# Kernel optimization log

Measured on AMD Instinct MI355X. Metric: run time of the kernel, lower is better.

The kernel has to match this reference:

```python
import jax, jax.numpy as jnp
import numpy as np

B, GEO_CH, SEM_CH, H, W = 8, 256, 256, 64, 64
HS, WS = 32, 32  # semantic branch spatial size
EPS_ATTN = 1e-6
EPS_GN = 1e-5


def _phi(x):
    return jax.nn.elu(x) + 1.0


def setup_inputs() -> dict:
    key = jax.random.key(0)
    ks = jax.random.split(key, 8)
    f_geo = jax.random.normal(ks[0], (B, GEO_CH, H, W), dtype=jnp.float32)
    f_sem = jax.random.normal(ks[1], (B, SEM_CH, HS, WS), dtype=jnp.float32)
    s = 0.02
    Wq = jax.random.normal(ks[2], (SEM_CH, GEO_CH), dtype=jnp.float32) * s
    Wk = jax.random.normal(ks[3], (SEM_CH, SEM_CH), dtype=jnp.float32) * s
    Wv = jax.random.normal(ks[4], (SEM_CH, SEM_CH), dtype=jnp.float32) * s
    Wo = jax.random.normal(ks[5], (GEO_CH, SEM_CH), dtype=jnp.float32) * s
    bq = jnp.zeros((SEM_CH,), jnp.float32)
    bk = jnp.zeros((SEM_CH,), jnp.float32)
    bv = jnp.zeros((SEM_CH,), jnp.float32)
    bo = jnp.zeros((GEO_CH,), jnp.float32)
    gn_w = jnp.ones((GEO_CH,), jnp.float32)
    gn_b = jnp.zeros((GEO_CH,), jnp.float32)
    return {"f_geo": f_geo, "f_sem": f_sem, "Wq": Wq, "bq": bq, "Wk": Wk,
            "bk": bk, "Wv": Wv, "bv": bv, "Wo": Wo, "bo": bo,
            "gn_w": gn_w, "gn_b": gn_b}


def _conv1x1(x, Wm, b):
    # x: [B,Cin,H,W], Wm: [Cout,Cin] -> [B,Cout,H,W]
    return jnp.einsum('oc,bchw->bohw', Wm, x) + b[None, :, None, None]


def reference(f_geo, f_sem, Wq, bq, Wk, bk, Wv, bv, Wo, bo, gn_w, gn_b):
    b, cg, h, w = f_geo.shape
    n = h * w
    # bilinear resize, half-pixel centers == torch align_corners=False
    f_sem_r = jax.image.resize(f_sem, (b, f_sem.shape[1], h, w), method='bilinear')
    Q = _phi(_conv1x1(f_geo, Wq, bq)).reshape(b, -1, n)      # [B,Cs,N]
    K = _phi(_conv1x1(f_sem_r, Wk, bk)).reshape(b, -1, n)    # [B,Cs,N]
    V = _conv1x1(f_sem_r, Wv, bv).reshape(b, -1, n)          # [B,Cs,N]
    KV = jnp.einsum('bcn,bdn->bcd', K, V)                    # [B,Cs,Cs]
    QKV = jnp.einsum('bcn,bcd->bnd', Q, KV)                  # [B,N,Cs]
    K_sum = K.sum(axis=-1)                                   # [B,Cs]
    norm = jnp.einsum('bcn,bc->bn', Q, K_sum)[..., None] + EPS_ATTN  # [B,N,1]
    out = (QKV / norm).transpose(0, 2, 1).reshape(b, -1, h, w)
    y = f_geo + _conv1x1(out, Wo, bo)
    # GroupNorm(1, geo_ch): normalize over (C,H,W) per sample, per-channel affine
    mu = y.mean(axis=(1, 2, 3), keepdims=True)
    var = y.var(axis=(1, 2, 3), keepdims=True)
    yn = (y - mu) * jax.lax.rsqrt(var + EPS_GN)
    return yn * gn_w[None, :, None, None] + gn_b[None, :, None, None]
```

## Files before the change

kernel.cpp:

```cpp
#include <hip/hip_runtime.h>
#include <hip/hip_bf16.h>


#define B_ 8
#define C_ 256
#define N_ 4096
#define NS_ 1024
#define KVCH 16

typedef unsigned short u16;
using bf16x8 = __attribute__((ext_vector_type(8))) short;
using f32x4 = __attribute__((ext_vector_type(4))) float;

__device__ inline u16 f2bf(float f) {
  unsigned u = __builtin_bit_cast(unsigned, f);
  unsigned r = (u + 0x7fffu + ((u >> 16) & 1u)) >> 16;
  return (u16)r;
}
__device__ inline float bf2f(u16 x) {
  return __builtin_bit_cast(float, ((unsigned)x) << 16);
}

__device__ __forceinline__ void gl_lds16(const u16* g, u16* l) {
  __builtin_amdgcn_global_load_lds((const __attribute__((address_space(1))) void*)g,
                                   (__attribute__((address_space(3))) void*)l, 16, 0, 0);
}

__device__ inline void gemm128_nt(const u16* __restrict__ At, const u16* __restrict__ Bt,
                                  int lda, int ldb, int k0, int k1,
                                  u16* __restrict__ lds, f32x4 acc[4][4])
{
  const int t = threadIdx.x;
  const int lane = t & 63, wave = t >> 6;
  const int wr = wave >> 1, wc = wave & 1;
  const int lr = lane & 15, lg = lane >> 4;
  const int sr = t >> 2, skv = (t & 3) * 8;
  u16* Ab = lds;
  u16* Bb = lds + 128 * 32;
  const u16* gA0 = At + (size_t)sr * lda + skv;
  const u16* gA1 = At + (size_t)(sr + 64) * lda + skv;
  const u16* gB0 = Bt + (size_t)sr * ldb + skv;
  const u16* gB1 = Bt + (size_t)(sr + 64) * ldb + skv;
  u16* dA0 = Ab + wave * 512;
  u16* dA1 = Ab + 2048 + wave * 512;
  u16* dB0 = Bb + wave * 512;
  u16* dB1 = Bb + 2048 + wave * 512;
  const u16* ap = Ab + (wr * 64 + lr) * 32 + lg * 8;
  const u16* bp = Bb + (wc * 64 + lr) * 32 + lg * 8;
  for (int k = k0; k < k1; k += 32) {
    gl_lds16(gA0 + k, dA0);
    gl_lds16(gA1 + k, dA1);
    gl_lds16(gB0 + k, dB0);
    gl_lds16(gB1 + k, dB1);
    __syncthreads();
    bf16x8 af[4], bfr[4];
#pragma unroll
    for (int i = 0; i < 4; ++i) af[i] = *reinterpret_cast<const bf16x8*>(ap + i * 16 * 32);
#pragma unroll
    for (int i = 0; i < 4; ++i) bfr[i] = *reinterpret_cast<const bf16x8*>(bp + i * 16 * 32);
#pragma unroll
    for (int m = 0; m < 4; ++m)
#pragma unroll
      for (int n = 0; n < 4; ++n)
        acc[m][n] = __builtin_amdgcn_mfma_f32_16x16x32_bf16(af[m], bfr[n], acc[m][n], 0, 0, 0);
    __syncthreads();
  }
}

__device__ inline void zero_acc4(f32x4 acc[4][4]) {
#pragma unroll
  for (int m = 0; m < 4; ++m)
#pragma unroll
    for (int n = 0; n < 4; ++n)
#pragma unroll
      for (int r = 0; r < 4; ++r) acc[m][n][r] = 0.f;
}

__device__ inline void ep_stage_half(const f32x4 acc[4][4], float* eplds, int h,
                                     int wr, int wc, int lr, int lg)
{
  if (wr == h) {
#pragma unroll
    for (int m = 0; m < 4; ++m)
#pragma unroll
      for (int n = 0; n < 4; ++n)
#pragma unroll
        for (int r = 0; r < 4; ++r)
          eplds[(m * 16 + lg * 4 + r) * 132 + wc * 64 + n * 16 + lr] = acc[m][n][r];
  }
}

__global__ __launch_bounds__(256) void k_transpose_cast(const float* __restrict__ in,
                                                        u16* __restrict__ out, int rows, int cols)
{
  __shared__ float tile[32][33];
  int b = blockIdx.z;
  const float* src = in + (size_t)b * rows * cols;
  u16* dst = out + (size_t)b * rows * cols;
  int c0 = blockIdx.x * 32, r0 = blockIdx.y * 32;
  int tx = threadIdx.x & 31, ty = threadIdx.x >> 5;
#pragma unroll
  for (int i = 0; i < 32; i += 8)
    tile[ty + i][tx] = src[(size_t)(r0 + ty + i) * cols + (c0 + tx)];
  __syncthreads();
#pragma unroll
  for (int i = 0; i < 32; i += 8)
    dst[(size_t)(c0 + ty + i) * rows + (r0 + tx)] = f2bf(tile[tx][ty + i]);
}

__global__ __launch_bounds__(256) void k_cast3(const float* __restrict__ wq, const float* __restrict__ wk,
                                               const float* __restrict__ wo,
                                               u16* oq, u16* ok, u16* oo,
                                               const float* __restrict__ bv, float* __restrict__ bov,
                                               float* __restrict__ stats)
{
  int i = blockIdx.x * 256 + threadIdx.x;
  oq[i] = f2bf(wq[i]); ok[i] = f2bf(wk[i]); oo[i] = f2bf(wo[i]);
  if (i < 16) stats[i] = 0.f;
  if (blockIdx.x == 255) {
    int o = threadIdx.x;
    float s = 0.f;
    for (int d = 0; d < C_; ++d) s += wo[o * C_ + d] * bv[d];
    bov[o] = s;
  }
}

__global__ __launch_bounds__(256) void k_wov(const u16* __restrict__ Wob, const u16* __restrict__ WvT,
                                             u16* __restrict__ Wov)
{
  __shared__ u16 glds[2 * 128 * 32];
  __shared__ float eplds[64 * 132];
  int tn = blockIdx.x, tm = blockIdx.y;
  const u16* A = Wob + (size_t)tm * 128 * C_;
  const u16* Bm = WvT + (size_t)tn * 128 * C_;
  f32x4 acc[4][4];
  zero_acc4(acc);
  gemm128_nt(A, Bm, C_, C_, 0, C_, glds, acc);
  int t = threadIdx.x, lane = t & 63, wave = t >> 6;
  int wr = wave >> 1, wc = wave & 1, lr = lane & 15, lg = lane >> 4;
  for (int h = 0; h < 2; ++h) {
    __syncthreads();
    ep_stage_half(acc, eplds, h, wr, wc, lr, lg);
    __syncthreads();
#pragma unroll
    for (int p = 0; p < 4; ++p) {
      int rloc = p * 8 + (t >> 5), cloc = (t & 31) * 4;
      int row = tm * 128 + h * 64 + rloc;
      float4 a = *(const float4*)&eplds[rloc * 132 + cloc];
      ushort4 o;
      o.x = f2bf(a.x); o.y = f2bf(a.y); o.z = f2bf(a.z); o.w = f2bf(a.w);
      *(ushort4*)&Wov[(size_t)row * C_ + tn * 128 + cloc] = o;
    }
  }
}

__global__ __launch_bounds__(256) void k_semconv(const u16* __restrict__ fsemT,
                                                 const u16* __restrict__ Wk, const u16* __restrict__ Wov,
                                                 const float* __restrict__ bk, const float* __restrict__ bov,
                                                 u16* __restrict__ Kpre, u16* __restrict__ V2pre)
{
  __shared__ u16 glds[2 * 128 * 32];
  __shared__ float eplds[64 * 132];
  int b = blockIdx.z >> 1, sel = blockIdx.z & 1;
  int m0 = blockIdx.y * 128, n0 = blockIdx.x * 128;
  const u16* A = (sel ? Wov : Wk) + (size_t)m0 * C_;
  const u16* Bm = fsemT + (size_t)b * NS_ * C_ + (size_t)n0 * C_;
  const float* bias = sel ? bov : bk;
  u16* out = (sel ? V2pre : Kpre) + (size_t)b * C_ * NS_;
  f32x4 acc[4][4];
  zero_acc4(acc);
  gemm128_nt(A, Bm, C_, C_, 0, C_, glds, acc);
  int t = threadIdx.x, lane = t & 63, wave = t >> 6;
  int wr = wave >> 1, wc = wave & 1, lr = lane & 15, lg = lane >> 4;
  for (int h = 0; h < 2; ++h) {
    __syncthreads();
    ep_stage_half(acc, eplds, h, wr, wc, lr, lg);
    __syncthreads();
#pragma unroll
    for (int p = 0; p < 4; ++p) {
      int rloc = p * 8 + (t >> 5), cloc = (t & 31) * 4;
      int row = m0 + h * 64 + rloc;
      float4 a = *(const float4*)&eplds[rloc * 132 + cloc];
      float bi = bias[row];
      ushort4 o;
      o.x = f2bf(a.x + bi); o.y = f2bf(a.y + bi); o.z = f2bf(a.z + bi); o.w = f2bf(a.w + bi);
      *(ushort4*)&out[(size_t)row * NS_ + n0 + cloc] = o;
    }
  }
}

__global__ __launch_bounds__(256) void k_resize(const u16* __restrict__ Kpre, const u16* __restrict__ V2pre,
                                                u16* __restrict__ Kbf, u16* __restrict__ V2bf,
                                                float* __restrict__ Ksum)
{
  int sel = blockIdx.y;
  const u16* src = (sel ? V2pre : Kpre) + (size_t)blockIdx.x * NS_;
  u16* dst = (sel ? V2bf : Kbf) + (size_t)blockIdx.x * N_;
  float s = 0.f;
  for (int i = threadIdx.x; i < N_; i += 256) {
    int yy = i >> 6, xx = i & 63;
    int yh = yy >> 1, xh = xx >> 1;
    int ys0, ys1, xs0, xs1; float wy0, wy1, wx0, wx1;
    if (yy & 1) { ys0 = yh; ys1 = yh < 31 ? yh + 1 : 31; wy0 = 0.75f; wy1 = 0.25f; }
    else        { ys0 = yh > 0 ? yh - 1 : 0; ys1 = yh;   wy0 = 0.25f; wy1 = 0.75f; }
    if (xx & 1) { xs0 = xh; xs1 = xh < 31 ? xh + 1 : 31; wx0 = 0.75f; wx1 = 0.25f; }
    else        { xs0 = xh > 0 ? xh - 1 : 0; xs1 = xh;   wx0 = 0.25f; wx1 = 0.75f; }
    float r0 = wx0 * bf2f(src[ys0 * 32 + xs0]) + wx1 * bf2f(src[ys0 * 32 + xs1]);
    float r1 = wx0 * bf2f(src[ys1 * 32 + xs0]) + wx1 * bf2f(src[ys1 * 32 + xs1]);
    float v = wy0 * r0 + wy1 * r1;
    if (!sel) { v = v > 0.f ? v + 1.f : __expf(v); s += v; }
    dst[i] = f2bf(v);
  }
  if (!sel) {
    __shared__ float red[256];
    red[threadIdx.x] = s; __syncthreads();
    for (int off = 128; off > 0; off >>= 1) {
      if (threadIdx.x < off) red[threadIdx.x] += red[threadIdx.x + off];
      __syncthreads();
    }
    if (threadIdx.x == 0) Ksum[blockIdx.x] = red[0];
  }
}

__global__ __launch_bounds__(256) void k_kv(const u16* __restrict__ V2bf, const u16* __restrict__ Kbf,
                                            float* __restrict__ Mpart)
{
  __shared__ u16 glds[2 * 128 * 32];
  __shared__ float eplds[64 * 132];
  int tn = blockIdx.x, tm = blockIdx.y;
  int b = blockIdx.z >> 4, ch = blockIdx.z & 15;
  const int kspan = N_ / KVCH;
  const u16* A = V2bf + (size_t)b * C_ * N_ + (size_t)tm * 128 * N_;
  const u16* Bm = Kbf + (size_t)b * C_ * N_ + (size_t)tn * 128 * N_;
  f32x4 acc[4][4];
  zero_acc4(acc);
  gemm128_nt(A, Bm, N_, N_, ch * kspan, ch * kspan + kspan, glds, acc);
  float* out = Mpart + ((size_t)(b * KVCH + ch) * 4 + tm * 2 + tn) * (128 * 128);
  int t = threadIdx.x, lane = t & 63, wave = t >> 6;
  int wr = wave >> 1, wc = wave & 1, lr = lane & 15, lg = lane >> 4;
  for (int h = 0; h < 2; ++h) {
    __syncthreads();
    ep_stage_half(acc, eplds, h, wr, wc, lr, lg);
    __syncthreads();
#pragma unroll
    for (int p = 0; p < 4; ++p) {
      int rloc = p * 8 + (t >> 5), cloc = (t & 31) * 4;
      float4 a = *(const float4*)&eplds[rloc * 132 + cloc];
      *(float4*)&out[(size_t)(h * 64 + rloc) * 128 + cloc] = a;
    }
    __syncthreads();
  }
}

__global__ __launch_bounds__(256) void k_kvred(const float* __restrict__ Mpart, u16* __restrict__ Mbf)
{
  int idx = blockIdx.x * 256 + threadIdx.x;
  int b = idx >> 16, cd = idx & 65535;
  int o = cd >> 8, c = cd & 255;
  int tile = ((o >> 7) << 1) + (c >> 7);
  int loc = (o & 127) * 128 + (c & 127);
  float s = 0.f;
#pragma unroll
  for (int ch = 0; ch < KVCH; ++ch)
    s += Mpart[((size_t)(b * KVCH + ch) * 4 + tile) * 16384 + loc];
  Mbf[idx] = f2bf(s);
}

__global__ __launch_bounds__(256) void k_fuse(const u16* __restrict__ fgeoT, const u16* __restrict__ Wqb,
                                              const float* __restrict__ bq, const float* __restrict__ Ksum,
                                              const u16* __restrict__ Mbf,
                                              const float* __restrict__ fgeo, const float* __restrict__ bo,
                                              float* __restrict__ y, float* __restrict__ stats)
{
  __shared__ u16 Qlds[64 * 264];
  __shared__ float normLds[64];
  __shared__ u16 stage[4096];
  __shared__ float eplds[32 * 68];
  const int t = threadIdx.x, lane = t & 63, wave = t >> 6;
  const int wr = wave >> 1, wc = wave & 1;
  const int lr = lane & 15, lg = lane >> 4;
  const int sr = t >> 2, skv = (t & 3) * 8;
  const int n0 = blockIdx.x * 64, b = blockIdx.y;
  if (t < 64) normLds[t] = 1e-6f;

  const u16* gA1 = fgeoT + (size_t)b * N_ * C_ + (size_t)(n0 + sr) * C_ + skv;
  for (int cc = 0; cc < 4; ++cc) {
    f32x4 a1[2][2];
#pragma unroll
    for (int m = 0; m < 2; ++m)
#pragma unroll
      for (int n = 0; n < 2; ++n)
#pragma unroll
        for (int r = 0; r < 4; ++r) a1[m][n][r] = 0.f;
    const u16* gB1 = Wqb + (size_t)(cc * 64 + sr) * C_ + skv;
    for (int k = 0; k < C_; k += 32) {
      gl_lds16(gA1 + k, stage + wave * 512);
      gl_lds16(gB1 + k, stage + 2048 + wave * 512);
      __syncthreads();
      const u16* ap = stage + (wr * 32 + lr) * 32 + lg * 8;
      const u16* bp = stage + 2048 + (wc * 32 + lr) * 32 + lg * 8;
      bf16x8 af[2], bfr[2];
#pragma unroll
      for (int i = 0; i < 2; ++i) af[i] = *(const bf16x8*)(ap + i * 16 * 32);
#pragma unroll
      for (int i = 0; i < 2; ++i) bfr[i] = *(const bf16x8*)(bp + i * 16 * 32);
#pragma unroll
      for (int m = 0; m < 2; ++m)
#pragma unroll
        for (int n = 0; n < 2; ++n)
          a1[m][n] = __builtin_amdgcn_mfma_f32_16x16x32_bf16(af[m], bfr[n], a1[m][n], 0, 0, 0);
      __syncthreads();
    }
#pragma unroll
    for (int m = 0; m < 2; ++m)
#pragma unroll
      for (int r = 0; r < 4; ++r) {
        int rown = wr * 32 + m * 16 + lg * 4 + r;
        float pn = 0.f;
#pragma unroll
        for (int n = 0; n < 2; ++n) {
          int colg = cc * 64 + wc * 32 + n * 16 + lr;
          float v = a1[m][n][r] + bq[colg];
          v = v > 0.f ? v + 1.f : __expf(v);
          Qlds[rown * 264 + colg] = f2bf(v);
          pn += v * Ksum[b * C_ + colg];
        }
        pn += __shfl_xor(pn, 1); pn += __shfl_xor(pn, 2);
        pn += __shfl_xor(pn, 4); pn += __shfl_xor(pn, 8);
        if (lr == 0) atomicAdd(&normLds[rown], pn);
      }
  }

  const float* fg = fgeo + (size_t)b * C_ * N_;
  float* yb = y + (size_t)b * C_ * N_;
  float ssum = 0.f, ssq = 0.f;
  for (int oh = 0; oh < 2; ++oh) {
    f32x4 a2[4][2];
#pragma unroll
    for (int m = 0; m < 4; ++m)
#pragma unroll
      for (int n = 0; n < 2; ++n)
#pragma unroll
        for (int r = 0; r < 4; ++r) a2[m][n][r] = 0.f;
    const u16* gM = Mbf + (size_t)b * C_ * C_ + (size_t)(oh * 128 + sr) * C_ + skv;
    for (int k = 0; k < C_; k += 32) {
      gl_lds16(gM + k, stage + wave * 512);
      gl_lds16(gM + (size_t)64 * C_ + k, stage + 2048 + wave * 512);
      __syncthreads();
      const u16* ap = stage + (wr * 64 + lr) * 32 + lg * 8;
      bf16x8 af[4], bfr[2];
#pragma unroll
      for (int i = 0; i < 4; ++i) af[i] = *(const bf16x8*)(ap + i * 16 * 32);
#pragma unroll
      for (int i = 0; i < 2; ++i)
        bfr[i] = *(const bf16x8*)&Qlds[(wc * 32 + i * 16 + lr) * 264 + k + lg * 8];
#pragma unroll
      for (int m = 0; m < 4; ++m)
#pragma unroll
        for (int n = 0; n < 2; ++n)
          a2[m][n] = __builtin_amdgcn_mfma_f32_16x16x32_bf16(af[m], bfr[n], a2[m][n], 0, 0, 0);
      __syncthreads();
    }
    for (int q = 0; q < 4; ++q) {
      __syncthreads();
      if (wr == (q >> 1)) {
        int m0 = (q & 1) * 2;
#pragma unroll
        for (int mm = 0; mm < 2; ++mm)
#pragma unroll
          for (int n = 0; n < 2; ++n)
#pragma unroll
            for (int r = 0; r < 4; ++r)
              eplds[(mm * 16 + lg * 4 + r) * 68 + wc * 32 + n * 16 + lr] = a2[m0 + mm][n][r];
      }
      __syncthreads();
#pragma unroll
      for (int p = 0; p < 2; ++p) {
        int rloc = p * 16 + (t >> 4), cloc = (t & 15) * 4;
        int o = oh * 128 + q * 32 + rloc;
        float4 a = *(const float4*)&eplds[rloc * 68 + cloc];
        float4 nv = *(const float4*)&normLds[cloc];
        float4 f = *(const float4*)&fg[(size_t)o * N_ + n0 + cloc];
        float bov = bo[o];
        float4 v;
        v.x = f.x + bov + a.x / nv.x;
        v.y = f.y + bov + a.y / nv.y;
        v.z = f.z + bov + a.z / nv.z;
        v.w = f.w + bov + a.w / nv.w;
        *(float4*)&yb[(size_t)o * N_ + n0 + cloc] = v;
        ssum += v.x + v.y + v.z + v.w;
        ssq += v.x * v.x + v.y * v.y + v.z * v.z + v.w * v.w;
      }
    }
  }
#pragma unroll
  for (int off = 1; off < 64; off <<= 1) {
    ssum += __shfl_xor(ssum, off);
    ssq += __shfl_xor(ssq, off);
  }
  if (lane == 0) {
    atomicAdd(&stats[b * 2], ssum);
    atomicAdd(&stats[b * 2 + 1], ssq);
  }
}

__global__ __launch_bounds__(256) void k_gn(float* __restrict__ y, const float* __restrict__ stats,
                                            const float* __restrict__ gnw, const float* __restrict__ gnb)
{
  int idx = blockIdx.x * 256 + threadIdx.x;
  int elem = idx * 8;
  int b = elem >> 20;
  int o = (elem >> 12) & 255;
  const float cnt = (float)C_ * (float)N_;
  float mu = stats[b * 2] / cnt;
  float var = stats[b * 2 + 1] / cnt - mu * mu;
  float rs = rsqrtf(var + 1e-5f);
  float sc = gnw[o] * rs;
  float sh = gnb[o] - mu * sc;
  float4* p = reinterpret_cast<float4*>(y) + idx * 2;
  float4 v0 = p[0], v1 = p[1];
  v0.x = v0.x * sc + sh; v0.y = v0.y * sc + sh; v0.z = v0.z * sc + sh; v0.w = v0.w * sc + sh;
  v1.x = v1.x * sc + sh; v1.y = v1.y * sc + sh; v1.z = v1.z * sc + sh; v1.w = v1.w * sc + sh;
  p[0] = v0; p[1] = v1;
}

extern "C" void kernel_launch(void* const* d_in, const int* in_sizes, int n_in,
                              void* d_out, int out_size, void* d_ws, size_t ws_size,
                              hipStream_t stream)
{
  const float* f_geo = (const float*)d_in[0];
  const float* f_sem = (const float*)d_in[1];
  const float* Wq = (const float*)d_in[2];
  const float* bq = (const float*)d_in[3];
  const float* Wk = (const float*)d_in[4];
  const float* bk = (const float*)d_in[5];
  const float* Wv = (const float*)d_in[6];
  const float* bv = (const float*)d_in[7];
  const float* Wo = (const float*)d_in[8];
  const float* bo = (const float*)d_in[9];
  const float* gnw = (const float*)d_in[10];
  const float* gnb = (const float*)d_in[11];
  float* y = (float*)d_out;

  char* w = (char*)d_ws;
  auto alloc = [&](size_t bytes) { char* p = w; w += (bytes + 255) & ~(size_t)255; return p; };
  u16* fsemT = (u16*)alloc((size_t)B_ * NS_ * C_ * 2);
  u16* fgeoT = (u16*)alloc((size_t)B_ * N_ * C_ * 2);
  u16* Wqb = (u16*)alloc(65536 * 2);
  u16* Wkb = (u16*)alloc(65536 * 2);
  u16* Wob = (u16*)alloc(65536 * 2);
  u16* WvT = (u16*)alloc(65536 * 2);
  u16* Wov = (u16*)alloc(65536 * 2);
  float* bov = (float*)alloc(C_ * 4);
  u16* Kpre = (u16*)alloc((size_t)B_ * C_ * NS_ * 2);
  u16* V2pre = (u16*)alloc((size_t)B_ * C_ * NS_ * 2);
  u16* Kbf = (u16*)alloc((size_t)B_ * C_ * N_ * 2);
  u16* V2bf = (u16*)alloc((size_t)B_ * C_ * N_ * 2);
  float* Ksum = (float*)alloc((size_t)B_ * C_ * 4);
  float* Mpart = (float*)alloc((size_t)B_ * KVCH * 4 * 16384 * 4);
  u16* Mbf = (u16*)alloc((size_t)B_ * C_ * C_ * 2);
  float* stats = (float*)alloc(256);

  k_transpose_cast<<<dim3(NS_ / 32, C_ / 32, B_), 256, 0, stream>>>(f_sem, fsemT, C_, NS_);
  k_transpose_cast<<<dim3(N_ / 32, C_ / 32, B_), 256, 0, stream>>>(f_geo, fgeoT, C_, N_);
  k_transpose_cast<<<dim3(C_ / 32, C_ / 32, 1), 256, 0, stream>>>(Wv, WvT, C_, C_);
  k_cast3<<<dim3(256), 256, 0, stream>>>(Wq, Wk, Wo, Wqb, Wkb, Wob, bv, bov, stats);
  k_wov<<<dim3(2, 2), 256, 0, stream>>>(Wob, WvT, Wov);
  k_semconv<<<dim3(8, 2, 16), 256, 0, stream>>>(fsemT, Wkb, Wov, bk, bov, Kpre, V2pre);
  k_resize<<<dim3(B_ * C_, 2), 256, 0, stream>>>(Kpre, V2pre, Kbf, V2bf, Ksum);
  k_kv<<<dim3(2, 2, B_ * KVCH), 256, 0, stream>>>(V2bf, Kbf, Mpart);
  k_kvred<<<dim3(2048), 256, 0, stream>>>(Mpart, Mbf);
  k_fuse<<<dim3(N_ / 64, B_), 256, 0, stream>>>(fgeoT, Wqb, bq, Ksum, Mbf, f_geo, bo, y, stats);
  k_gn<<<dim3(B_ * C_ * N_ / 8 / 256), 256, 0, stream>>>(y, stats, gnw, gnb);
}
```

Before: 277.2 us.

## Shrink GEMM tiles to 64x64 with deeper K staging and retile fused attention kernel

Replaces the 128x128 GEMM helper with a 64x64 tile that stages 128-wide K slabs per barrier. k_wov, k_semconv and k_kv are relaunched with four times more blocks, and their LDS is aliased between staging and epilogue. k_kvred is vectorized with float4. k_fuse now works on 32-pixel tiles, keeps the Q operand fragments in registers and streams Wq and M in 32-row chunks, aiming for more parallelism and fewer barriers at the cost of more redundant weight loads per block.

New measurement: 322.8 us. +16.4%, slower.

```diff
diff --git a/kernel.cpp b/kernel.cpp
--- a/kernel.cpp
+++ b/kernel.cpp
@@ -20,73 +20,44 @@
 __device__ inline float bf2f(u16 x) {
   return __builtin_bit_cast(float, ((unsigned)x) << 16);
 }
-
 __device__ __forceinline__ void gl_lds16(const u16* g, u16* l) {
   __builtin_amdgcn_global_load_lds((const __attribute__((address_space(1))) void*)g,
                                    (__attribute__((address_space(3))) void*)l, 16, 0, 0);
 }
 
-__device__ inline void gemm128_nt(const u16* __restrict__ At, const u16* __restrict__ Bt,
-                                  int lda, int ldb, int k0, int k1,
-                                  u16* __restrict__ lds, f32x4 acc[4][4])
-{
-  const int t = threadIdx.x;
-  const int lane = t & 63, wave = t >> 6;
-  const int wr = wave >> 1, wc = wave & 1;
-  const int lr = lane & 15, lg = lane >> 4;
-  const int sr = t >> 2, skv = (t & 3) * 8;
-  u16* Ab = lds;
-  u16* Bb = lds + 128 * 32;
-  const u16* gA0 = At + (size_t)sr * lda + skv;
-  const u16* gA1 = At + (size_t)(sr + 64) * lda + skv;
-  const u16* gB0 = Bt + (size_t)sr * ldb + skv;
-  const u16* gB1 = Bt + (size_t)(sr + 64) * ldb + skv;
-  u16* dA0 = Ab + wave * 512;
-  u16* dA1 = Ab + 2048 + wave * 512;
-  u16* dB0 = Bb + wave * 512;
-  u16* dB1 = Bb + 2048 + wave * 512;
-  const u16* ap = Ab + (wr * 64 + lr) * 32 + lg * 8;
-  const u16* bp = Bb + (wc * 64 + lr) * 32 + lg * 8;
-  for (int k = k0; k < k1; k += 32) {
-    gl_lds16(gA0 + k, dA0);
-    gl_lds16(gA1 + k, dA1);
-    gl_lds16(gB0 + k, dB0);
-    gl_lds16(gB1 + k, dB1);
+__device__ inline void gemm64(const u16* __restrict__ A, const u16* __restrict__ Bm,
+                              int lda, int ldb, int k0,
+                              u16* __restrict__ lds, f32x4 (&acc)[2][2])
+{
+  const int t = threadIdx.x, lane = t & 63, w = t >> 6;
+  const int wr = w >> 1, wc = w & 1, lr = lane & 15;
+  const int lg = lane >> 4;
+  const int srow = w * 16 + (lane >> 2), scol = (lane & 3) * 8;
+  u16* Alds = lds;
+  u16* Blds = lds + 8192;
+  for (int slab = 0; slab < 2; ++slab) {
+    const int kb = k0 + slab * 128;
+#pragma unroll
+    for (int i = 0; i < 4; ++i)
+      gl_lds16(A + (size_t)srow * lda + kb + i * 32 + scol, Alds + i * 2048 + w * 512);
+#pragma unroll
+    for (int i = 0; i < 4; ++i)
+      gl_lds16(Bm + (size_t)srow * ldb + kb + i * 32 + scol, Blds + i * 2048 + w * 512);
     __syncthreads();
-    bf16x8 af[4], bfr[4];
-#pragma unroll
-    for (int i = 0; i < 4; ++i) af[i] = *reinterpret_cast<const bf16x8*>(ap + i * 16 * 32);
-#pragma unroll
-    for (int i = 0; i < 4; ++i) bfr[i] = *reinterpret_cast<const bf16x8*>(bp + i * 16 * 32);
-#pragma unroll
-    for (int m = 0; m < 4; ++m)
-#pragma unroll
-      for (int n = 0; n < 4; ++n)
-        acc[m][n] = __builtin_amdgcn_mfma_f32_16x16x32_bf16(af[m], bfr[n], acc[m][n], 0, 0, 0);
+#pragma unroll
+    for (int ch = 0; ch < 4; ++ch) {
+      const u16* ap = Alds + ch * 2048 + (wr * 32 + lr) * 32 + lg * 8;
+      const u16* bp = Blds + ch * 2048 + (wc * 32 + lr) * 32 + lg * 8;
+      bf16x8 af[2], bf[2];
+      af[0] = *(const bf16x8*)ap; af[1] = *(const bf16x8*)(ap + 16 * 32);
+      bf[0] = *(const bf16x8*)bp; bf[1] = *(const bf16x8*)(bp + 16 * 32);
+#pragma unroll
+      for (int m = 0; m < 2; ++m)
+#pragma unroll
+        for (int n = 0; n < 2; ++n)
+          acc[m][n] = __builtin_amdgcn_mfma_f32_16x16x32_bf16(af[m], bf[n], acc[m][n], 0, 0, 0);
+    }
     __syncthreads();
-  }
-}
-
-__device__ inline void zero_acc4(f32x4 acc[4][4]) {
-#pragma unroll
-  for (int m = 0; m < 4; ++m)
-#pragma unroll
-    for (int n = 0; n < 4; ++n)
-#pragma unroll
-      for (int r = 0; r < 4; ++r) acc[m][n][r] = 0.f;
-}
-
-__device__ inline void ep_stage_half(const f32x4 acc[4][4], float* eplds, int h,
-                                     int wr, int wc, int lr, int lg)
-{
-  if (wr == h) {
-#pragma unroll
-    for (int m = 0; m < 4; ++m)
-#pragma unroll
-      for (int n = 0; n < 4; ++n)
-#pragma unroll
-        for (int r = 0; r < 4; ++r)
-          eplds[(m * 16 + lg * 4 + r) * 132 + wc * 64 + n * 16 + lr] = acc[m][n][r];
   }
 }
 
@@ -128,29 +99,29 @@
 __global__ __launch_bounds__(256) void k_wov(const u16* __restrict__ Wob, const u16* __restrict__ WvT,
                                              u16* __restrict__ Wov)
 {
-  __shared__ u16 glds[2 * 128 * 32];
-  __shared__ float eplds[64 * 132];
+  __shared__ __align__(16) char smem[32768];
+  u16* glds = (u16*)smem;
+  float* eplds = (float*)smem;
   int tn = blockIdx.x, tm = blockIdx.y;
-  const u16* A = Wob + (size_t)tm * 128 * C_;
-  const u16* Bm = WvT + (size_t)tn * 128 * C_;
-  f32x4 acc[4][4];
-  zero_acc4(acc);
-  gemm128_nt(A, Bm, C_, C_, 0, C_, glds, acc);
-  int t = threadIdx.x, lane = t & 63, wave = t >> 6;
-  int wr = wave >> 1, wc = wave & 1, lr = lane & 15, lg = lane >> 4;
-  for (int h = 0; h < 2; ++h) {
-    __syncthreads();
-    ep_stage_half(acc, eplds, h, wr, wc, lr, lg);
-    __syncthreads();
-#pragma unroll
-    for (int p = 0; p < 4; ++p) {
-      int rloc = p * 8 + (t >> 5), cloc = (t & 31) * 4;
-      int row = tm * 128 + h * 64 + rloc;
-      float4 a = *(const float4*)&eplds[rloc * 132 + cloc];
-      ushort4 o;
-      o.x = f2bf(a.x); o.y = f2bf(a.y); o.z = f2bf(a.z); o.w = f2bf(a.w);
-      *(ushort4*)&Wov[(size_t)row * C_ + tn * 128 + cloc] = o;
-    }
+  f32x4 acc[2][2] = {};
+  gemm64(Wob + (size_t)tm * 64 * C_, WvT + (size_t)tn * 64 * C_, C_, C_, 0, glds, acc);
+  int t = threadIdx.x, lane = t & 63, w = t >> 6;
+  int wr = w >> 1, wc = w & 1, lr = lane & 15, lg = lane >> 4;
+#pragma unroll
+  for (int m = 0; m < 2; ++m)
+#pragma unroll
+    for (int n = 0; n < 2; ++n)
+#pragma unroll
+      for (int r = 0; r < 4; ++r)
+        eplds[(wr * 32 + m * 16 + lg * 4 + r) * 68 + wc * 32 + n * 16 + lr] = acc[m][n][r];
+  __syncthreads();
+#pragma unroll
+  for (int rd = 0; rd < 4; ++rd) {
+    int rloc = rd * 16 + (t >> 4), cloc = (t & 15) * 4;
+    float4 a = *(const float4*)&eplds[rloc * 68 + cloc];
+    ushort4 o;
+    o.x = f2bf(a.x); o.y = f2bf(a.y); o.z = f2bf(a.z); o.w = f2bf(a.w);
+    *(ushort4*)&Wov[(size_t)(tm * 64 + rloc) * C_ + tn * 64 + cloc] = o;
   }
 }
 
@@ -159,33 +130,36 @@
                                                  const float* __restrict__ bk, const float* __restrict__ bov,
                                                  u16* __restrict__ Kpre, u16* __restrict__ V2pre)
 {
-  __shared__ u16 glds[2 * 128 * 32];
-  __shared__ float eplds[64 * 132];
+  __shared__ __align__(16) char smem[32768];
+  u16* glds = (u16*)smem;
+  float* eplds = (float*)smem;
   int b = blockIdx.z >> 1, sel = blockIdx.z & 1;
-  int m0 = blockIdx.y * 128, n0 = blockIdx.x * 128;
+  int m0 = blockIdx.y * 64, n0 = blockIdx.x * 64;
   const u16* A = (sel ? Wov : Wk) + (size_t)m0 * C_;
   const u16* Bm = fsemT + (size_t)b * NS_ * C_ + (size_t)n0 * C_;
   const float* bias = sel ? bov : bk;
   u16* out = (sel ? V2pre : Kpre) + (size_t)b * C_ * NS_;
-  f32x4 acc[4][4];
-  zero_acc4(acc);
-  gemm128_nt(A, Bm, C_, C_, 0, C_, glds, acc);
-  int t = threadIdx.x, lane = t & 63, wave = t >> 6;
-  int wr = wave >> 1, wc = wave & 1, lr = lane & 15, lg = lane >> 4;
-  for (int h = 0; h < 2; ++h) {
-    __syncthreads();
-    ep_stage_half(acc, eplds, h, wr, wc, lr, lg);
-    __syncthreads();
-#pragma unroll
-    for (int p = 0; p < 4; ++p) {
-      int rloc = p * 8 + (t >> 5), cloc = (t & 31) * 4;
-      int row = m0 + h * 64 + rloc;
-      float4 a = *(const float4*)&eplds[rloc * 132 + cloc];
-      float bi = bias[row];
-      ushort4 o;
-      o.x = f2bf(a.x + bi); o.y = f2bf(a.y + bi); o.z = f2bf(a.z + bi); o.w = f2bf(a.w + bi);
-      *(ushort4*)&out[(size_t)row * NS_ + n0 + cloc] = o;
-    }
+  f32x4 acc[2][2] = {};
+  gemm64(A, Bm, C_, C_, 0, glds, acc);
+  int t = threadIdx.x, lane = t & 63, w = t >> 6;
+  int wr = w >> 1, wc = w & 1, lr = lane & 15, lg = lane >> 4;
+#pragma unroll
+  for (int m = 0; m < 2; ++m)
+#pragma unroll
+    for (int n = 0; n < 2; ++n)
+#pragma unroll
+      for (int r = 0; r < 4; ++r)
+        eplds[(wr * 32 + m * 16 + lg * 4 + r) * 68 + wc * 32 + n * 16 + lr] = acc[m][n][r];
+  __syncthreads();
+#pragma unroll
+  for (int rd = 0; rd < 4; ++rd) {
+    int rloc = rd * 16 + (t >> 4), cloc = (t & 15) * 4;
+    int row = m0 + rloc;
+    float4 a = *(const float4*)&eplds[rloc * 68 + cloc];
+    float bi = bias[row];
+    ushort4 o;
+    o.x = f2bf(a.x + bi); o.y = f2bf(a.y + bi); o.z = f2bf(a.z + bi); o.w = f2bf(a.w + bi);
+    *(ushort4*)&out[(size_t)row * NS_ + n0 + cloc] = o;
   }
 }
 
@@ -225,45 +199,53 @@
 __global__ __launch_bounds__(256) void k_kv(const u16* __restrict__ V2bf, const u16* __restrict__ Kbf,
                                             float* __restrict__ Mpart)
 {
-  __shared__ u16 glds[2 * 128 * 32];
-  __shared__ float eplds[64 * 132];
+  __shared__ __align__(16) char smem[32768];
+  u16* glds = (u16*)smem;
+  float* eplds = (float*)smem;
   int tn = blockIdx.x, tm = blockIdx.y;
   int b = blockIdx.z >> 4, ch = blockIdx.z & 15;
-  const int kspan = N_ / KVCH;
-  const u16* A = V2bf + (size_t)b * C_ * N_ + (size_t)tm * 128 * N_;
-  const u16* Bm = Kbf + (size_t)b * C_ * N_ + (size_t)tn * 128 * N_;
-  f32x4 acc[4][4];
-  zero_acc4(acc);
-  gemm128_nt(A, Bm, N_, N_, ch * kspan, ch * kspan + kspan, glds, acc);
-  float* out = Mpart + ((size_t)(b * KVCH + ch) * 4 + tm * 2 + tn) * (128 * 128);
-  int t = threadIdx.x, lane = t & 63, wave = t >> 6;
-  int wr = wave >> 1, wc = wave & 1, lr = lane & 15, lg = lane >> 4;
-  for (int h = 0; h < 2; ++h) {
-    __syncthreads();
-    ep_stage_half(acc, eplds, h, wr, wc, lr, lg);
-    __syncthreads();
-#pragma unroll
-    for (int p = 0; p < 4; ++p) {
-      int rloc = p * 8 + (t >> 5), cloc = (t & 31) * 4;
-      float4 a = *(const float4*)&eplds[rloc * 132 + cloc];
-      *(float4*)&out[(size_t)(h * 64 + rloc) * 128 + cloc] = a;
-    }
-    __syncthreads();
+  const u16* A = V2bf + (size_t)b * C_ * N_ + (size_t)tm * 64 * N_;
+  const u16* Bm = Kbf + (size_t)b * C_ * N_ + (size_t)tn * 64 * N_;
+  f32x4 acc[2][2] = {};
+  gemm64(A, Bm, N_, N_, ch * 256, glds, acc);
+  float* out = Mpart + ((size_t)(b * 16 + ch) * 16 + tm * 4 + tn) * 4096;
+  int t = threadIdx.x, lane = t & 63, w = t >> 6;
+  int wr = w >> 1, wc = w & 1, lr = lane & 15, lg = lane >> 4;
+#pragma unroll
+  for (int m = 0; m < 2; ++m)
+#pragma unroll
+    for (int n = 0; n < 2; ++n)
+#pragma unroll
+      for (int r = 0; r < 4; ++r)
+        eplds[(wr * 32 + m * 16 + lg * 4 + r) * 68 + wc * 32 + n * 16 + lr] = acc[m][n][r];
+  __syncthreads();
+#pragma unroll
+  for (int rd = 0; rd < 4; ++rd) {
+    int rloc = rd * 16 + (t >> 4), cloc = (t & 15) * 4;
+    float4 a = *(const float4*)&eplds[rloc * 68 + cloc];
+    *(float4*)&out[rloc * 64 + cloc] = a;
   }
 }
 
 __global__ __launch_bounds__(256) void k_kvred(const float* __restrict__ Mpart, u16* __restrict__ Mbf)
 {
-  int idx = blockIdx.x * 256 + threadIdx.x;
-  int b = idx >> 16, cd = idx & 65535;
-  int o = cd >> 8, c = cd & 255;
-  int tile = ((o >> 7) << 1) + (c >> 7);
-  int loc = (o & 127) * 128 + (c & 127);
-  float s = 0.f;
-#pragma unroll
-  for (int ch = 0; ch < KVCH; ++ch)
-    s += Mpart[((size_t)(b * KVCH + ch) * 4 + tile) * 16384 + loc];
-  Mbf[idx] = f2bf(s);
+  int q = blockIdx.x * 256 + threadIdx.x;
+  int b = q >> 14;
+  int rem = q & 16383;
+  int o = rem >> 6;
+  int c0 = (rem & 63) * 4;
+  int tile = ((o >> 6) << 2) + (c0 >> 6);
+  int loc = (o & 63) * 64 + (c0 & 63);
+  const float* base = Mpart + (size_t)b * 16 * 16 * 4096 + (size_t)tile * 4096 + loc;
+  float4 s = {0.f, 0.f, 0.f, 0.f};
+#pragma unroll
+  for (int ch = 0; ch < KVCH; ++ch) {
+    float4 v = *(const float4*)(base + (size_t)ch * 16 * 4096);
+    s.x += v.x; s.y += v.y; s.z += v.z; s.w += v.w;
+  }
+  ushort4 out;
+  out.x = f2bf(s.x); out.y = f2bf(s.y); out.z = f2bf(s.z); out.w = f2bf(s.w);
+  *(ushort4*)&Mbf[(size_t)q * 4] = out;
 }
 
 __global__ __launch_bounds__(256) void k_fuse(const u16* __restrict__ fgeoT, const u16* __restrict__ Wqb,
@@ -272,125 +254,104 @@
                                               const float* __restrict__ fgeo, const float* __restrict__ bo,
                                               float* __restrict__ y, float* __restrict__ stats)
 {
-  __shared__ u16 Qlds[64 * 264];
-  __shared__ float normLds[64];
-  __shared__ u16 stage[4096];
-  __shared__ float eplds[32 * 68];
-  const int t = threadIdx.x, lane = t & 63, wave = t >> 6;
-  const int wr = wave >> 1, wc = wave & 1;
-  const int lr = lane & 15, lg = lane >> 4;
-  const int sr = t >> 2, skv = (t & 3) * 8;
-  const int n0 = blockIdx.x * 64, b = blockIdx.y;
-  if (t < 64) normLds[t] = 1e-6f;
-
-  const u16* gA1 = fgeoT + (size_t)b * N_ * C_ + (size_t)(n0 + sr) * C_ + skv;
-  for (int cc = 0; cc < 4; ++cc) {
-    f32x4 a1[2][2];
-#pragma unroll
-    for (int m = 0; m < 2; ++m)
-#pragma unroll
-      for (int n = 0; n < 2; ++n)
-#pragma unroll
-        for (int r = 0; r < 4; ++r) a1[m][n][r] = 0.f;
-    const u16* gB1 = Wqb + (size_t)(cc * 64 + sr) * C_ + skv;
-    for (int k = 0; k < C_; k += 32) {
-      gl_lds16(gA1 + k, stage + wave * 512);
-      gl_lds16(gB1 + k, stage + 2048 + wave * 512);
+  __shared__ __align__(16) char smem[66688];
+  u16* Qlds = (u16*)smem;
+  u16* Ast = (u16*)(smem + 33792);
+  u16* Bst = (u16*)(smem + 50176);
+  float* normLds = (float*)(smem + 66560);
+  float* eplds = (float*)(smem + 33792);
+  const int t = threadIdx.x, lane = t & 63, w = t >> 6;
+  const int wr = w >> 1, wc = w & 1, lr = lane & 15, lg = lane >> 4;
+  const int sr2 = (w & 1) * 16 + (lane >> 2);
+  const int sch2 = w >> 1;
+  const int scol = (lane & 3) * 8;
+  const int n0 = blockIdx.x * 32, b = blockIdx.y;
+  if (t < 32) normLds[t] = 1e-6f;
+
+  auto stage32 = [&](const u16* g, u16* dst) {
+#pragma unroll
+    for (int i = 0; i < 4; ++i)
+      gl_lds16(g + (size_t)sr2 * C_ + (2 * i + sch2) * 32 + scol, dst + i * 2048 + w * 512);
+  };
+
+  stage32(fgeoT + (size_t)b * N_ * C_ + (size_t)n0 * C_, Ast);
+  stage32(Wqb, Bst);
+  __syncthreads();
+
+  float bqv[8], ksv[8];
+#pragma unroll
+  for (int cc = 0; cc < 8; ++cc) {
+    int c = cc * 32 + wc * 16 + lr;
+    bqv[cc] = bq[c];
+    ksv[cc] = Ksum[b * C_ + c];
+  }
+  bf16x8 af[8];
+#pragma unroll
+  for (int ch = 0; ch < 8; ++ch)
+    af[ch] = *(const bf16x8*)(Ast + ch * 1024 + (wr * 16 + lr) * 32 + lg * 8);
+
+  for (int cc = 0; cc < 8; ++cc) {
+    f32x4 a1 = {0.f, 0.f, 0.f, 0.f};
+#pragma unroll
+    for (int ch = 0; ch < 8; ++ch) {
+      bf16x8 bf = *(const bf16x8*)(Bst + ch * 1024 + (wc * 16 + lr) * 32 + lg * 8);
+      a1 = __builtin_amdgcn_mfma_f32_16x16x32_bf16(af[ch], bf, a1, 0, 0, 0);
+    }
+#pragma unroll
+    for (int rr = 0; rr < 4; ++rr) {
+      int n = wr * 16 + lg * 4 + rr;
+      float v = a1[rr] + bqv[cc];
+      v = v > 0.f ? v + 1.f : __expf(v);
+      Qlds[n * 264 + cc * 32 + wc * 16 + lr] = f2bf(v);
+      float pn = v * ksv[cc];
+      pn += __shfl_xor(pn, 1); pn += __shfl_xor(pn, 2);
+      pn += __shfl_xor(pn, 4); pn += __shfl_xor(pn, 8);
+      if (lr == 0) atomicAdd(&normLds[n], pn);
+    }
+    __syncthreads();
+    if (cc < 7) {
+      stage32(Wqb + (size_t)(cc + 1) * 32 * C_, Bst);
       __syncthreads();
-      const u16* ap = stage + (wr * 32 + lr) * 32 + lg * 8;
-      const u16* bp = stage + 2048 + (wc * 32 + lr) * 32 + lg * 8;
-      bf16x8 af[2], bfr[2];
-#pragma unroll
-      for (int i = 0; i < 2; ++i) af[i] = *(const bf16x8*)(ap + i * 16 * 32);
-#pragma unroll
-      for (int i = 0; i < 2; ++i) bfr[i] = *(const bf16x8*)(bp + i * 16 * 32);
-#pragma unroll
-      for (int m = 0; m < 2; ++m)
-#pragma unroll
-        for (int n = 0; n < 2; ++n)
-          a1[m][n] = __builtin_amdgcn_mfma_f32_16x16x32_bf16(af[m], bfr[n], a1[m][n], 0, 0, 0);
-      __syncthreads();
-    }
-#pragma unroll
-    for (int m = 0; m < 2; ++m)
-#pragma unroll
-      for (int r = 0; r < 4; ++r) {
-        int rown = wr * 32 + m * 16 + lg * 4 + r;
-        float pn = 0.f;
-#pragma unroll
-        for (int n = 0; n < 2; ++n) {
-          int colg = cc * 64 + wc * 32 + n * 16 + lr;
-          float v = a1[m][n][r] + bq[colg];
-          v = v > 0.f ? v + 1.f : __expf(v);
-          Qlds[rown * 264 + colg] = f2bf(v);
-          pn += v * Ksum[b * C_ + colg];
-        }
-        pn += __shfl_xor(pn, 1); pn += __shfl_xor(pn, 2);
-        pn += __shfl_xor(pn, 4); pn += __shfl_xor(pn, 8);
-        if (lr == 0) atomicAdd(&normLds[rown], pn);
-      }
-  }
+    }
+  }
+
+  __syncthreads();
+  bf16x8 qf[8];
+#pragma unroll
+  for (int ch = 0; ch < 8; ++ch)
+    qf[ch] = *(const bf16x8*)&Qlds[(wc * 16 + lr) * 264 + ch * 32 + lg * 8];
 
   const float* fg = fgeo + (size_t)b * C_ * N_;
   float* yb = y + (size_t)b * C_ * N_;
   float ssum = 0.f, ssq = 0.f;
-  for (int oh = 0; oh < 2; ++oh) {
-    f32x4 a2[4][2];
-#pragma unroll
-    for (int m = 0; m < 4; ++m)
-#pragma unroll
-      for (int n = 0; n < 2; ++n)
-#pragma unroll
-        for (int r = 0; r < 4; ++r) a2[m][n][r] = 0.f;
-    const u16* gM = Mbf + (size_t)b * C_ * C_ + (size_t)(oh * 128 + sr) * C_ + skv;
-    for (int k = 0; k < C_; k += 32) {
-      gl_lds16(gM + k, stage + wave * 512);
-      gl_lds16(gM + (size_t)64 * C_ + k, stage + 2048 + wave * 512);
-      __syncthreads();
-      const u16* ap = stage + (wr * 64 + lr) * 32 + lg * 8;
-      bf16x8 af[4], bfr[2];
-#pragma unroll
-      for (int i = 0; i < 4; ++i) af[i] = *(const bf16x8*)(ap + i * 16 * 32);
-#pragma unroll
-      for (int i = 0; i < 2; ++i)
-        bfr[i] = *(const bf16x8*)&Qlds[(wc * 32 + i * 16 + lr) * 264 + k + lg * 8];
-#pragma unroll
-      for (int m = 0; m < 4; ++m)
-#pragma unroll
-        for (int n = 0; n < 2; ++n)
-          a2[m][n] = __builtin_amdgcn_mfma_f32_16x16x32_bf16(af[m], bfr[n], a2[m][n], 0, 0, 0);
-      __syncthreads();
-    }
-    for (int q = 0; q < 4; ++q) {
-      __syncthreads();
-      if (wr == (q >> 1)) {
-        int m0 = (q & 1) * 2;
-#pragma unroll
-        for (int mm = 0; mm < 2; ++mm)
-#pragma unroll
-          for (int n = 0; n < 2; ++n)
-#pragma unroll
-            for (int r = 0; r < 4; ++r)
-              eplds[(mm * 16 + lg * 4 + r) * 68 + wc * 32 + n * 16 + lr] = a2[m0 + mm][n][r];
-      }
-      __syncthreads();
-#pragma unroll
-      for (int p = 0; p < 2; ++p) {
-        int rloc = p * 16 + (t >> 4), cloc = (t & 15) * 4;
-        int o = oh * 128 + q * 32 + rloc;
-        float4 a = *(const float4*)&eplds[rloc * 68 + cloc];
-        float4 nv = *(const float4*)&normLds[cloc];
-        float4 f = *(const float4*)&fg[(size_t)o * N_ + n0 + cloc];
-        float bov = bo[o];
-        float4 v;
-        v.x = f.x + bov + a.x / nv.x;
-        v.y = f.y + bov + a.y / nv.y;
-        v.z = f.z + bov + a.z / nv.z;
-        v.w = f.w + bov + a.w / nv.w;
-        *(float4*)&yb[(size_t)o * N_ + n0 + cloc] = v;
-        ssum += v.x + v.y + v.z + v.w;
-        ssq += v.x * v.x + v.y * v.y + v.z * v.z + v.w * v.w;
-      }
+  for (int oh = 0; oh < 8; ++oh) {
+    stage32(Mbf + (size_t)b * C_ * C_ + (size_t)oh * 32 * C_, Bst);
+    __syncthreads();
+    f32x4 a2 = {0.f, 0.f, 0.f, 0.f};
+#pragma unroll
+    for (int ch = 0; ch < 8; ++ch) {
+      bf16x8 mf = *(const bf16x8*)(Bst + ch * 1024 + (wr * 16 + lr) * 32 + lg * 8);
+      a2 = __builtin_amdgcn_mfma_f32_16x16x32_bf16(mf, qf[ch], a2, 0, 0, 0);
+    }
+#pragma unroll
+    for (int rr = 0; rr < 4; ++rr)
+      eplds[(wr * 16 + lg * 4 + rr) * 36 + wc * 16 + lr] = a2[rr];
+    __syncthreads();
+    {
+      int rloc = t >> 3, cloc = (t & 7) * 4;
+      int o = oh * 32 + rloc;
+      float4 a = *(const float4*)&eplds[rloc * 36 + cloc];
+      float4 nv = *(const float4*)&normLds[cloc];
+      float4 f = *(const float4*)&fg[(size_t)o * N_ + n0 + cloc];
+      float bov2 = bo[o];
+      float4 v;
+      v.x = f.x + bov2 + a.x / nv.x;
+      v.y = f.y + bov2 + a.y / nv.y;
+      v.z = f.z + bov2 + a.z / nv.z;
+      v.w = f.w + bov2 + a.w / nv.w;
+      *(float4*)&yb[(size_t)o * N_ + n0 + cloc] = v;
+      ssum += v.x + v.y + v.z + v.w;
+      ssq += v.x * v.x + v.y * v.y + v.z * v.z + v.w * v.w;
     }
   }
 #pragma unroll
@@ -457,7 +418,7 @@
   u16* Kbf = (u16*)alloc((size_t)B_ * C_ * N_ * 2);
   u16* V2bf = (u16*)alloc((size_t)B_ * C_ * N_ * 2);
   float* Ksum = (float*)alloc((size_t)B_ * C_ * 4);
-  float* Mpart = (float*)alloc((size_t)B_ * KVCH * 4 * 16384 * 4);
+  float* Mpart = (float*)alloc((size_t)B_ * 16 * 16 * 4096 * 4);
   u16* Mbf = (u16*)alloc((size_t)B_ * C_ * C_ * 2);
   float* stats = (float*)alloc(256);
 
@@ -465,11 +426,11 @@
   k_transpose_cast<<<dim3(N_ / 32, C_ / 32, B_), 256, 0, stream>>>(f_geo, fgeoT, C_, N_);
   k_transpose_cast<<<dim3(C_ / 32, C_ / 32, 1), 256, 0, stream>>>(Wv, WvT, C_, C_);
   k_cast3<<<dim3(256), 256, 0, stream>>>(Wq, Wk, Wo, Wqb, Wkb, Wob, bv, bov, stats);
-  k_wov<<<dim3(2, 2), 256, 0, stream>>>(Wob, WvT, Wov);
-  k_semconv<<<dim3(8, 2, 16), 256, 0, stream>>>(fsemT, Wkb, Wov, bk, bov, Kpre, V2pre);
+  k_wov<<<dim3(4, 4), 256, 0, stream>>>(Wob, WvT, Wov);
+  k_semconv<<<dim3(16, 4, 16), 256, 0, stream>>>(fsemT, Wkb, Wov, bk, bov, Kpre, V2pre);
   k_resize<<<dim3(B_ * C_, 2), 256, 0, stream>>>(Kpre, V2pre, Kbf, V2bf, Ksum);
-  k_kv<<<dim3(2, 2, B_ * KVCH), 256, 0, stream>>>(V2bf, Kbf, Mpart);
-  k_kvred<<<dim3(2048), 256, 0, stream>>>(Mpart, Mbf);
-  k_fuse<<<dim3(N_ / 64, B_), 256, 0, stream>>>(fgeoT, Wqb, bq, Ksum, Mbf, f_geo, bo, y, stats);
+  k_kv<<<dim3(4, 4, B_ * 16), 256, 0, stream>>>(V2bf, Kbf, Mpart);
+  k_kvred<<<dim3(512), 256, 0, stream>>>(Mpart, Mbf);
+  k_fuse<<<dim3(N_ / 32, B_), 256, 0, stream>>>(fgeoT, Wqb, bq, Ksum, Mbf, f_geo, bo, y, stats);
   k_gn<<<dim3(B_ * C_ * N_ / 8 / 256), 256, 0, stream>>>(y, stats, gnw, gnb);
 }
```
